# Kernel optimization log

Hardware: AMD Instinct MI355X
Metric: run time of the kernel (lower is better)

Reference implementation:

```python
import jax, jax.numpy as jnp
import numpy as np
from jax import lax

DIVISOR = 2.0

def setup_inputs() -> dict:
    key = jax.random.key(0)
    k1, k2, k3, k4 = jax.random.split(key, 4)
    x = jax.random.normal(k1, (32, 3, 32, 128, 128), dtype=jnp.float16)
    conv_w = jax.random.normal(k2, (16, 3, 3, 3, 3), dtype=jnp.float16) * 0.1
    conv_b = jax.random.normal(k3, (16,), dtype=jnp.float16)
    bias = jax.random.normal(k4, (16,), dtype=jnp.float16)
    return {"x": x, "conv_w": conv_w, "conv_b": conv_b, "bias": bias}

def reference(x, conv_w, conv_b, bias):
    # Conv3d (valid padding, stride 1), fp16 like conv.half()
    y = lax.conv_general_dilated(
        x, conv_w, window_strides=(1, 1, 1), padding="VALID",
        dimension_numbers=("NCDHW", "OIDHW", "NCDHW"))
    y = y + conv_b[None, :, None, None, None]
    # Fused ReLU + 2x2x2 max pool
    y = jnp.maximum(y, jnp.asarray(0, y.dtype))
    B, C, D, H, W = y.shape
    Dp, Hp, Wp = D // 2, H // 2, W // 2
    pooled = y[:, :, :2 * Dp, :2 * Hp, :2 * Wp].reshape(
        B, C, Dp, 2, Hp, 2, Wp, 2).max(axis=(3, 5, 7))  # [B,C,Dp,Hp,Wp]
    # Spatial mean in fp32 (kernel accumulates in float)
    avg = pooled.astype(jnp.float32).mean(axis=(2, 3, 4))  # [B,C]
    # /divisor + bias[c], then sum over channels -> [B,1,1,1]
    per_ch = avg / DIVISOR + bias.astype(jnp.float32)[None, :]
    return per_ch.sum(axis=1).reshape(B, 1, 1, 1)
```

## Files before the change

### kernel.cpp

```cpp
#include <hip/hip_runtime.h>
#include <hip/hip_bf16.h>


typedef __attribute__((ext_vector_type(8)))  short  short8;
typedef __attribute__((ext_vector_type(4)))  float  floatx4;
typedef __attribute__((ext_vector_type(16))) float  floatx16;

__device__ __forceinline__ short f2bf(float f) {
    unsigned u = __builtin_bit_cast(unsigned, f);
    unsigned r = (u + 0x7FFFu + ((u >> 16) & 1u)) >> 16;
    return (short)r;
}

__device__ __forceinline__ unsigned pkbf2(float a, float b) {
    __hip_bfloat162 h = __float22bfloat162_rn(float2{a, b});
    unsigned r;
    __builtin_memcpy(&r, &h, 4);
    return r;
}

__global__ void init_kernel(const float* __restrict__ wg,
                            const float* __restrict__ biasg,
                            short* __restrict__ wtab,
                            float* __restrict__ out)
{
    const int t = threadIdx.x;
    if (t < 576) {
        const int lane = t & 63, f = t >> 6;
        const int kh = f / 3, kw = f % 3;
        const int m = lane & 31, hs = lane >> 5;
        const int dd = m >> 4, ch = m & 15;
        short8 v;
        #pragma unroll
        for (int j = 0; j < 8; ++j) {
            const int s = hs * 8 + j;
            const int ci = s >> 2, dl = s & 3;
            const int kd = dl - dd;
            v[j] = (ci < 3 && kd >= 0 && kd < 3)
                 ? f2bf(wg[ch * 81 + ci * 27 + kd * 9 + kh * 3 + kw]) : (short)0;
        }
        ((short8*)wtab)[f * 64 + lane] = v;
    }
    if (t < 32) {
        float s = 0.f;
        #pragma unroll
        for (int cc = 0; cc < 16; ++cc) s += biasg[cc];
        out[t] = s;
    }
}

__global__ __launch_bounds__(512, 4) void fused_conv_pool_reduce(
    const float* __restrict__ xg,
    const short* __restrict__ wtab,
    const float* __restrict__ cbg,
    float* __restrict__ out)
{
    __shared__ __align__(16) short rawT[130 * 64];
    __shared__ float wsums[8];

    const int hp  = blockIdx.x;
    const int b   = blockIdx.y;
    const int tid = threadIdx.x;
    const int lane = tid & 63;
    const int wv   = tid >> 6;
    const int hs   = lane >> 5;

    short8 af[9];
    #pragma unroll
    for (int f = 0; f < 9; ++f) af[f] = ((const short8*)wtab)[f * 64 + lane];
    float cb8[8];
    #pragma unroll
    for (int r = 0; r < 8; ++r) cb8[r] = cbg[(r & 3) + 8 * (r >> 2) + 4 * hs];

    {
        const int row = tid >> 2, hl = tid & 3;
        const int phys = ((hl * 2 + 1) ^ ((row ^ (row >> 3)) & 7));
        *(unsigned long long*)((char*)rawT + row * 128 + phys * 16 + 8) = 0ULL;
    }
    if (tid < 32)
        *(unsigned long long*)((char*)rawT + 16384 + tid * 8) = 0ULL;

    const int w4 = tid & 31, hr = (tid >> 5) & 3, dr = (tid >> 7) & 3;
    int waddr[3][4];
    #pragma unroll
    for (int ci = 0; ci < 3; ++ci) {
        #pragma unroll
        for (int i = 0; i < 4; ++i) {
            const int row = 4 * w4 + i;
            const int phys = (hr * 2 + (ci >> 1)) ^ ((row ^ (row >> 3)) & 7);
            waddr[ci][i] = row * 128 + phys * 16 + ((ci * 4 + dr) & 7) * 2;
        }
    }
    const int wi = lane & 15, hh = (lane >> 4) & 1;
    int raddr[3][3];
    #pragma unroll
    for (int kh = 0; kh < 3; ++kh) {
        #pragma unroll
        for (int kw = 0; kw < 3; ++kw) {
            const int row = wv * 16 + wi + kw;
            const int phys = ((hh + kh) * 2 + hs) ^ ((row ^ (row >> 3)) & 7);
            raddr[kh][kw] = row * 128 + phys * 16;
        }
    }

    const float* src = xg + ((size_t)b * 96 + dr) * 16384 + (2 * hp + hr) * 128 + 4 * w4;
    floatx4 c0 = *(const floatx4*)(src);
    floatx4 c1 = *(const floatx4*)(src + 524288);
    floatx4 c2 = *(const floatx4*)(src + 1048576);

    float vsum = 0.f;
    for (int dp = 0; dp < 15; ++dp) {
        #pragma unroll
        for (int ci = 0; ci < 3; ++ci) {
            const floatx4 c = (ci == 0) ? c0 : (ci == 1) ? c1 : c2;
            const unsigned p0 = pkbf2(c[0], c[1]);
            const unsigned p1 = pkbf2(c[2], c[3]);
            *(short*)((char*)rawT + waddr[ci][0]) = (short)(p0 & 0xFFFF);
            *(short*)((char*)rawT + waddr[ci][1]) = (short)(p0 >> 16);
            *(short*)((char*)rawT + waddr[ci][2]) = (short)(p1 & 0xFFFF);
            *(short*)((char*)rawT + waddr[ci][3]) = (short)(p1 >> 16);
        }
        if (dp < 14) {
            src += 32768;
            c0 = *(const floatx4*)(src);
            c1 = *(const floatx4*)(src + 524288);
            c2 = *(const floatx4*)(src + 1048576);
        }
        __syncthreads();

        floatx16 acc = {0.f,0.f,0.f,0.f,0.f,0.f,0.f,0.f,
                        0.f,0.f,0.f,0.f,0.f,0.f,0.f,0.f};
        #pragma unroll
        for (int kh = 0; kh < 3; ++kh) {
            #pragma unroll
            for (int kw = 0; kw < 3; ++kw) {
                const short8 bf = *(const short8*)((char*)rawT + raddr[kh][kw]);
                acc = __builtin_amdgcn_mfma_f32_32x32x16_bf16(af[kh * 3 + kw], bf, acc, 0, 0, 0);
            }
        }
        #pragma unroll
        for (int r = 0; r < 8; ++r) {
            float v = fmaxf(fmaxf(acc[r], acc[r + 8]) + cb8[r], 0.f);
            v = fmaxf(v, __shfl_xor(v, 16, 64));
            v = fmaxf(v, __shfl_xor(v, 1, 64));
            vsum += v;
        }
        __syncthreads();
    }

    const bool okl = ((lane & 0x11) == 0) && (wv * 16 + (lane & 14) <= 124);
    float s = okl ? vsum : 0.f;
    #pragma unroll
    for (int off = 1; off < 64; off <<= 1) s += __shfl_xor(s, off, 64);

    if (lane == 0) wsums[wv] = s;
    __syncthreads();
    if (tid == 0) {
        float bs = 0.f;
        #pragma unroll
        for (int i = 0; i < 8; ++i) bs += wsums[i];
        atomicAdd(&out[b], bs * (1.0f / 119070.0f));
    }
}

extern "C" void kernel_launch(void* const* d_in, const int* in_sizes, int n_in,
                              void* d_out, int out_size, void* d_ws, size_t ws_size,
                              hipStream_t stream) {
    const float* x      = (const float*)d_in[0];
    const float* conv_w = (const float*)d_in[1];
    const float* conv_b = (const float*)d_in[2];
    const float* bias   = (const float*)d_in[3];
    float* out = (float*)d_out;
    short* wtab = (short*)d_ws;

    init_kernel<<<1, 576, 0, stream>>>(conv_w, bias, wtab, out);
    dim3 grid(63, 32);
    fused_conv_pool_reduce<<<grid, 512, 0, stream>>>(x, wtab, conv_b, out);
}
```

Measured before the change: 330.9 us.

## Double-buffer LDS tile, pack channels per write, use DPP for pool max

Double-buffers the shared-memory input tile so the second barrier per depth step can be dropped. The LDS layout is changed so one 8-byte store holds three input channels (with a zero pad) for a given depth row, replacing twelve 2-byte stores. The weight table and lane mapping are reordered to match, which lets the 2x2 pooling max use DPP quad permutes instead of ds_swizzle shuffles. This doubles LDS use per block, which could lower occupancy, and correctness depends on the remapped lane indexing being consistent.

```diff
diff --git a/kernel.cpp b/kernel.cpp
--- a/kernel.cpp
+++ b/kernel.cpp
@@ -19,6 +19,13 @@
     return r;
 }
 
+template <int CTRL>
+__device__ __forceinline__ float dpp_max(float v) {
+    int x = __builtin_bit_cast(int, v);
+    int y = __builtin_amdgcn_mov_dpp(x, CTRL, 0xF, 0xF, true);
+    return fmaxf(v, __builtin_bit_cast(float, y));
+}
+
 __global__ void init_kernel(const float* __restrict__ wg,
                             const float* __restrict__ biasg,
                             short* __restrict__ wtab,
@@ -34,7 +41,7 @@
         #pragma unroll
         for (int j = 0; j < 8; ++j) {
             const int s = hs * 8 + j;
-            const int ci = s >> 2, dl = s & 3;
+            const int dl = s >> 2, ci = s & 3;
             const int kd = dl - dd;
             v[j] = (ci < 3 && kd >= 0 && kd < 3)
                  ? f2bf(wg[ch * 81 + ci * 27 + kd * 9 + kh * 3 + kw]) : (short)0;
@@ -55,7 +62,7 @@
     const float* __restrict__ cbg,
     float* __restrict__ out)
 {
-    __shared__ __align__(16) short rawT[130 * 64];
+    __shared__ __align__(16) short rawT[2 * 130 * 64];
     __shared__ float wsums[8];
 
     const int hp  = blockIdx.x;
@@ -72,26 +79,21 @@
     #pragma unroll
     for (int r = 0; r < 8; ++r) cb8[r] = cbg[(r & 3) + 8 * (r >> 2) + 4 * hs];
 
+    if (tid < 64)
+        *(unsigned long long*)((char*)rawT + (tid >> 5) * 16640 + 16384 + (tid & 31) * 8) = 0ULL;
+
+    const int w4 = tid & 31, dr = (tid >> 5) & 3, hr = (tid >> 7) & 3;
+    int waddr[4];
     {
-        const int row = tid >> 2, hl = tid & 3;
-        const int phys = ((hl * 2 + 1) ^ ((row ^ (row >> 3)) & 7));
-        *(unsigned long long*)((char*)rawT + row * 128 + phys * 16 + 8) = 0ULL;
-    }
-    if (tid < 32)
-        *(unsigned long long*)((char*)rawT + 16384 + tid * 8) = 0ULL;
-
-    const int w4 = tid & 31, hr = (tid >> 5) & 3, dr = (tid >> 7) & 3;
-    int waddr[3][4];
-    #pragma unroll
-    for (int ci = 0; ci < 3; ++ci) {
+        const int chunkL = hr * 2 + (dr >> 1);
         #pragma unroll
         for (int i = 0; i < 4; ++i) {
             const int row = 4 * w4 + i;
-            const int phys = (hr * 2 + (ci >> 1)) ^ ((row ^ (row >> 3)) & 7);
-            waddr[ci][i] = row * 128 + phys * 16 + ((ci * 4 + dr) & 7) * 2;
+            const int phys = chunkL ^ ((row ^ (row >> 3)) & 7);
+            waddr[i] = row * 128 + phys * 16 + (dr & 1) * 8;
         }
     }
-    const int wi = lane & 15, hh = (lane >> 4) & 1;
+    const int wi = (lane >> 1) & 15, hh = lane & 1;
     int raddr[3][3];
     #pragma unroll
     for (int kh = 0; kh < 3; ++kh) {
@@ -110,15 +112,13 @@
 
     float vsum = 0.f;
     for (int dp = 0; dp < 15; ++dp) {
+        const int bofs = (dp & 1) * 16640;
         #pragma unroll
-        for (int ci = 0; ci < 3; ++ci) {
-            const floatx4 c = (ci == 0) ? c0 : (ci == 1) ? c1 : c2;
-            const unsigned p0 = pkbf2(c[0], c[1]);
-            const unsigned p1 = pkbf2(c[2], c[3]);
-            *(short*)((char*)rawT + waddr[ci][0]) = (short)(p0 & 0xFFFF);
-            *(short*)((char*)rawT + waddr[ci][1]) = (short)(p0 >> 16);
-            *(short*)((char*)rawT + waddr[ci][2]) = (short)(p1 & 0xFFFF);
-            *(short*)((char*)rawT + waddr[ci][3]) = (short)(p1 >> 16);
+        for (int i = 0; i < 4; ++i) {
+            uint2 pk;
+            pk.x = pkbf2(c0[i], c1[i]);
+            pk.y = pkbf2(c2[i], 0.0f);
+            *(uint2*)((char*)rawT + bofs + waddr[i]) = pk;
         }
         if (dp < 14) {
             src += 32768;
@@ -134,21 +134,20 @@
         for (int kh = 0; kh < 3; ++kh) {
             #pragma unroll
             for (int kw = 0; kw < 3; ++kw) {
-                const short8 bf = *(const short8*)((char*)rawT + raddr[kh][kw]);
+                const short8 bf = *(const short8*)((char*)rawT + bofs + raddr[kh][kw]);
                 acc = __builtin_amdgcn_mfma_f32_32x32x16_bf16(af[kh * 3 + kw], bf, acc, 0, 0, 0);
             }
         }
         #pragma unroll
         for (int r = 0; r < 8; ++r) {
             float v = fmaxf(fmaxf(acc[r], acc[r + 8]) + cb8[r], 0.f);
-            v = fmaxf(v, __shfl_xor(v, 16, 64));
-            v = fmaxf(v, __shfl_xor(v, 1, 64));
+            v = dpp_max<0xB1>(v);
+            v = dpp_max<0x4E>(v);
             vsum += v;
         }
-        __syncthreads();
     }
 
-    const bool okl = ((lane & 0x11) == 0) && (wv * 16 + (lane & 14) <= 124);
+    const bool okl = ((lane & 3) == 0) && (wv * 16 + wi <= 124);
     float s = okl ? vsum : 0.f;
     #pragma unroll
     for (int off = 1; off < 64; off <<= 1) s += __shfl_xor(s, off, 64);
```

Result: faster. 302.6 us (-8.6%).
